# Optimization experiments

Hardware: AMD Instinct MI355X
Metric: run time of the kernel (lower is better)

The kernel has to match this reference:

```python
import jax, jax.numpy as jnp
import numpy as np
from functools import partial

B = 256          # batch_size (== hidden_dim, required by the module's broadcasting)
T = 512          # seq_length
H = 256          # hidden_dim == dim_out
E = 6            # emb_dim
V = 10           # num_input_digits
C = 10           # num_classes


def _kaiming(key, shape):
    fan_in = shape[1]
    return jax.random.normal(key, shape, dtype=jnp.float32) * np.sqrt(2.0 / fan_in)


def setup_inputs() -> dict:
    key = jax.random.key(0)
    ks = jax.random.split(key, 12)
    inp = {
        "x": jax.random.randint(ks[0], (B, T), 0, V),
        "emb": jax.random.normal(ks[1], (V, E), dtype=jnp.float32),
        "Wxg": _kaiming(ks[2], (H, E)), "Whg": _kaiming(ks[3], (H, H)), "bg": jnp.zeros((H,), jnp.float32),
        "Wxi": _kaiming(ks[4], (H, E)), "Whi": _kaiming(ks[5], (H, H)), "bi": jnp.zeros((H,), jnp.float32),
        "Wxf": _kaiming(ks[6], (H, E)), "Whf": _kaiming(ks[7], (H, H)), "bf": jnp.zeros((H,), jnp.float32),
        "Wxo": _kaiming(ks[8], (H, E)), "Who": _kaiming(ks[9], (H, H)), "bo": jnp.zeros((H,), jnp.float32),
        "Wp": _kaiming(ks[10], (C, H)), "bp": jnp.zeros((C,), jnp.float32),
    }
    return inp


def reference(x, emb, Wxg, Whg, bg, Wxi, Whi, bi, Wxf, Whf, bf, Wxo, Who, bo, Wp, bp):
    # x: (B, T) int -> embed -> (B, T, E)
    xe = emb[x]
    # time-major (T, E, B): each step uses x_t.T as in the torch code
    xt_seq = jnp.transpose(xe, (1, 2, 0))

    h0 = jnp.zeros((H, B), jnp.float32)  # h lives as (H, B) per original math
    c0 = jnp.zeros((H, B), jnp.float32)

    def step(carry, xTt):  # xTt: (E, B)
        h, c = carry
        # NOTE: bias (H,) broadcasts over the trailing batch axis (H==B), faithful
        # to the original torch broadcasting.
        g = jnp.tanh(Wxg @ xTt + Whg @ h + bg)
        i = jax.nn.sigmoid(Wxi @ xTt + Whi @ h + bi)
        f = jax.nn.sigmoid(Wxf @ xTt + Whf @ h + bf)
        o = jax.nn.sigmoid(Wxo @ xTt + Who @ h + bo)
        c = g * i + c * f
        h = jnp.tanh(c) * o
        return (h, c), None

    (h, c), _ = jax.lax.scan(step, (h0, c0), xt_seq)
    return (Wp @ h).T + bp  # (B, C)
```

## Files before the change

### kernel.cpp

```cpp
#include <hip/hip_runtime.h>
#include <hip/hip_bf16.h>


typedef __attribute__((ext_vector_type(4))) int   int4v;
typedef __attribute__((ext_vector_type(4))) float float4v;

#define MFMA_I8(a, b, c) __builtin_amdgcn_mfma_i32_16x16x64_i8(a, b, c, 0, 0, 0)

#define K_TANH (-2.8853900817779268f)
#define K_SIG  (-1.4426950408889634f)

#define HSTRIDE 320

__device__ __forceinline__ short f2b(float f) {
    __hip_bfloat16 b = __float2bfloat16(f); return *(short*)&b;
}
__device__ __forceinline__ float b2f(short s) {
    union { unsigned int u; float f; } v; v.u = ((unsigned int)(unsigned short)s) << 16; return v.f;
}
__device__ __forceinline__ float fexp2(float x) {
#if __has_builtin(__builtin_amdgcn_exp2f)
    return __builtin_amdgcn_exp2f(x);
#else
    return __expf(x * 0.6931471805599453f);
#endif
}
__device__ __forceinline__ float frcp(float x) { return __builtin_amdgcn_rcpf(x); }

__global__ __attribute__((amdgpu_flat_work_group_size(1024, 1024), amdgpu_waves_per_eu(4, 4)))
void lstm_i8(
    const int* __restrict__ x,
    const float* __restrict__ emb,
    const float* __restrict__ Wxg, const float* __restrict__ Whg, const float* __restrict__ bg,
    const float* __restrict__ Wxi, const float* __restrict__ Whi, const float* __restrict__ bi,
    const float* __restrict__ Wxf, const float* __restrict__ Whf, const float* __restrict__ bff,
    const float* __restrict__ Wxo, const float* __restrict__ Who, const float* __restrict__ bo,
    const float* __restrict__ Wp, const float* __restrict__ bp,
    float* __restrict__ out)
{
    const int tid = threadIdx.x, bid = blockIdx.x;
    const int c0 = bid * 2;
    const int w = tid >> 6, lane = tid & 63;
    const int l = lane & 15, q = lane >> 4;
    const int col = l & 1;
    const int si  = (l >> 1) & 3;
    const int dup = (l >> 3) & 1;
    const int rw  = 16 * w;
    const int row = rw + 4 * q + si;

    __shared__ __align__(16) unsigned int hbuf[2][2 * HSTRIDE / 4];
    __shared__ __align__(16) short hfin[2 * 264];
    __shared__ unsigned char xdig2[512 * 2];
    __shared__ __align__(16) float tblC[2 * 10 * 1024];
    __shared__ float scaleL[4 * 256];

    const float* WxT[4] = {Wxg, Wxi, Wxf, Wxo};
    const float* WhT[4] = {Whg, Whi, Whf, Who};
    const float* bT[4]  = {bg, bi, bff, bo};

    if (tid < 2 * HSTRIDE / 4) hbuf[0][tid] = 0u;
    if (tid < 1024)
        xdig2[tid] = (unsigned char)x[(c0 + (tid & 1)) * 512 + (tid >> 1)];

    for (int i = tid; i < 5120; i += 1024) {
        int cc  = i / 2560;
        int rem = i - cc * 2560;
        int d = rem >> 8, r = rem & 255;
        float4v v;
        #pragma unroll
        for (int g = 0; g < 4; g++) {
            float s = 0.f;
            #pragma unroll
            for (int e = 0; e < 6; e++) s += WxT[g][r * 6 + e] * emb[d * 6 + e];
            v[g] = (s + bT[g][c0 + cc]) * (g == 0 ? K_TANH : K_SIG);
        }
        *(float4v*)&tblC[cc * 10240 + d * 1024 + r * 4] = v;
    }

    int4v wa[4][4];
    #pragma unroll
    for (int g = 0; g < 4; g++) {
        const float* Wr = WhT[g] + (rw + l) * 256 + q * 16;
        float mx = 0.f;
        #pragma unroll
        for (int kt = 0; kt < 4; kt++)
            #pragma unroll
            for (int c4 = 0; c4 < 4; c4++) {
                float4v v = *(const float4v*)(Wr + kt * 64 + c4 * 4);
                #pragma unroll
                for (int j = 0; j < 4; j++) mx = fmaxf(mx, fabsf(v[j]));
            }
        mx = fmaxf(mx, __shfl_xor(mx, 16));
        mx = fmaxf(mx, __shfl_xor(mx, 32));
        mx = fmaxf(mx, 1e-20f);
        if (q == 0) scaleL[g * 256 + rw + l] = mx;
        float qs = 127.f / mx;
        #pragma unroll
        for (int kt = 0; kt < 4; kt++) {
            int4v f;
            #pragma unroll
            for (int dw = 0; dw < 4; dw++) {
                float4v v = *(const float4v*)(Wr + kt * 64 + dw * 4);
                int word = 0;
                #pragma unroll
                for (int byt = 0; byt < 4; byt++) {
                    int z = (int)rintf(v[byt] * qs);
                    word |= (z & 255) << (8 * byt);
                }
                f[dw] = word;
            }
            wa[g][kt] = f;
        }
    }

    __syncthreads();

    float dscl[4];
    #pragma unroll
    for (int g = 0; g < 4; g++) {
        float kk = (g == 0 ? K_TANH : K_SIG) * (1.f / 16129.f);
        dscl[g] = scaleL[g * 256 + row] * kk;
    }

    const bool bi1 = (si & 1) != 0;
    const bool bi2 = (si & 2) != 0;
    const float* tprow = tblC + col * 10240 + row * 4;
    const int hoff = col * HSTRIDE + row;

    const int4v Z = {0, 0, 0, 0};

    float cs = 0.f, hl = 0.f;

    for (int t = 0; t < 512; t++) {
        const int p = t & 1;
        const char* hbase = (const char*)hbuf[p] + col * HSTRIDE + q * 16;

        int dg = xdig2[t * 2 + col];
        float4v tb = *(const float4v*)(tprow + dg * 1024);

        int4v hf0 = *(const int4v*)(hbase + 0 * 64);
        int4v hf1 = *(const int4v*)(hbase + 1 * 64);
        int4v hf2 = *(const int4v*)(hbase + 2 * 64);
        int4v hf3 = *(const int4v*)(hbase + 3 * 64);

        int4v ag = MFMA_I8(wa[0][0], hf0, Z);
        int4v ai = MFMA_I8(wa[1][0], hf0, Z);
        int4v af = MFMA_I8(wa[2][0], hf0, Z);
        int4v ao = MFMA_I8(wa[3][0], hf0, Z);
        ag = MFMA_I8(wa[0][1], hf1, ag);
        ai = MFMA_I8(wa[1][1], hf1, ai);
        af = MFMA_I8(wa[2][1], hf1, af);
        ao = MFMA_I8(wa[3][1], hf1, ao);
        ag = MFMA_I8(wa[0][2], hf2, ag);
        ai = MFMA_I8(wa[1][2], hf2, ai);
        af = MFMA_I8(wa[2][2], hf2, af);
        ao = MFMA_I8(wa[3][2], hf2, ao);

        ag = MFMA_I8(wa[0][3], hf3, ag);
        int avg_;
        { int s0 = bi1 ? ag[1] : ag[0]; int s1 = bi1 ? ag[3] : ag[2]; avg_ = bi2 ? s1 : s0; }
        float pg = fmaf((float)avg_, dscl[0], tb[0]);
        float Eg = fexp2(pg);

        ai = MFMA_I8(wa[1][3], hf3, ai);
        int avi_;
        { int s0 = bi1 ? ai[1] : ai[0]; int s1 = bi1 ? ai[3] : ai[2]; avi_ = bi2 ? s1 : s0; }
        float pi = fmaf((float)avi_, dscl[1], tb[1]);
        float Ei = fexp2(pi);
        float m1 = (1.f + Eg) * (1.f + Ei);

        af = MFMA_I8(wa[2][3], hf3, af);
        int avf_;
        { int s0 = bi1 ? af[1] : af[0]; int s1 = bi1 ? af[3] : af[2]; avf_ = bi2 ? s1 : s0; }
        float pf = fmaf((float)avf_, dscl[2], tb[2]);
        float Ef = fexp2(pf);
        float fp1 = 1.f + Ef;
        float num = fmaf(cs, m1, (1.f - Eg) * fp1);
        float c   = num * frcp(m1 * fp1);
        cs = c;
        float Ec = fexp2(K_TANH * c);

        ao = MFMA_I8(wa[3][3], hf3, ao);
        int avo_;
        { int s0 = bi1 ? ao[1] : ao[0]; int s1 = bi1 ? ao[3] : ao[2]; avo_ = bi2 ? s1 : s0; }
        float po = fmaf((float)avo_, dscl[3], tb[3]);
        float Eo = fexp2(po);
        float hh = (1.f - Ec) * frcp((1.f + Ec) * (1.f + Eo));
        hl = hh;
        if (dup == 0)
            *((char*)hbuf[1 - p] + hoff) = (char)((int)rintf(hh * 127.f));

        __syncthreads();
    }

    if (dup == 0) hfin[col * 264 + row] = f2b(hl);
    __syncthreads();

    if (tid < 20) {
        int pc = tid / 10, cls = tid - pc * 10;
        const short* hcol = &hfin[pc * 264];
        const float* wrow = Wp + cls * 256;
        float s = 0.f;
        #pragma unroll 8
        for (int k = 0; k < 256; k++) s += b2f(hcol[k]) * wrow[k];
        out[(c0 + pc) * 10 + cls] = s + bp[cls];
    }
}

extern "C" void kernel_launch(void* const* d_in, const int* in_sizes, int n_in,
                              void* d_out, int out_size, void* d_ws, size_t ws_size,
                              hipStream_t stream) {
    const int*   x   = (const int*)d_in[0];
    const float* emb = (const float*)d_in[1];
    const float* Wxg = (const float*)d_in[2];
    const float* Whg = (const float*)d_in[3];
    const float* bg  = (const float*)d_in[4];
    const float* Wxi = (const float*)d_in[5];
    const float* Whi = (const float*)d_in[6];
    const float* bi  = (const float*)d_in[7];
    const float* Wxf = (const float*)d_in[8];
    const float* Whf = (const float*)d_in[9];
    const float* bff = (const float*)d_in[10];
    const float* Wxo = (const float*)d_in[11];
    const float* Who = (const float*)d_in[12];
    const float* bo  = (const float*)d_in[13];
    const float* Wp  = (const float*)d_in[14];
    const float* bp  = (const float*)d_in[15];

    hipLaunchKernelGGL(lstm_i8, dim3(128), dim3(1024), 0, stream,
                       x, emb, Wxg, Whg, bg, Wxi, Whi, bi, Wxf, Whf, bff,
                       Wxo, Who, bo, Wp, bp, (float*)d_out);
}
```

Measured before the change: 553.6 us.

## Halve workgroup to 8 waves with two row tiles per wave, prefetch input table

Each wave now computes two 16-row tiles of the gate matrices, so the block drops from 16 to 8 waves and every lane produces a unique output. The old layout had half the lanes duplicating work. This cuts the number of waves taking part in the per-step barrier and removes the redundant elementwise lanes, in exchange for twice the MFMA chain per wave and twice the weight registers. The next step's input-projection table entry is also loaded ahead of time so its LDS latency overlaps the MFMAs.

```diff
diff --git a/kernel.cpp b/kernel.cpp
--- a/kernel.cpp
+++ b/kernel.cpp
@@ -27,7 +27,7 @@
 }
 __device__ __forceinline__ float frcp(float x) { return __builtin_amdgcn_rcpf(x); }
 
-__global__ __attribute__((amdgpu_flat_work_group_size(1024, 1024), amdgpu_waves_per_eu(4, 4)))
+__global__ __attribute__((amdgpu_flat_work_group_size(512, 512), amdgpu_waves_per_eu(2, 2)))
 void lstm_i8(
     const int* __restrict__ x,
     const float* __restrict__ emb,
@@ -42,11 +42,11 @@
     const int c0 = bid * 2;
     const int w = tid >> 6, lane = tid & 63;
     const int l = lane & 15, q = lane >> 4;
-    const int col = l & 1;
-    const int si  = (l >> 1) & 3;
-    const int dup = (l >> 3) & 1;
-    const int rw  = 16 * w;
-    const int row = rw + 4 * q + si;
+    const int col = lane & 1;
+    const int rtb = (lane >> 1) & 1;
+    const int si  = (lane >> 2) & 3;
+    const int rwb = 32 * w;
+    const int row = rwb + 16 * rtb + 4 * q + si;
 
     __shared__ __align__(16) unsigned int hbuf[2][2 * HSTRIDE / 4];
     __shared__ __align__(16) short hfin[2 * 264];
@@ -59,10 +59,10 @@
     const float* bT[4]  = {bg, bi, bff, bo};
 
     if (tid < 2 * HSTRIDE / 4) hbuf[0][tid] = 0u;
-    if (tid < 1024)
-        xdig2[tid] = (unsigned char)x[(c0 + (tid & 1)) * 512 + (tid >> 1)];
-
-    for (int i = tid; i < 5120; i += 1024) {
+    for (int i = tid; i < 1024; i += 512)
+        xdig2[i] = (unsigned char)x[(c0 + (i & 1)) * 512 + (i >> 1)];
+
+    for (int i = tid; i < 5120; i += 512) {
         int cc  = i / 2560;
         int rem = i - cc * 2560;
         int d = rem >> 8, r = rem & 255;
@@ -77,39 +77,42 @@
         *(float4v*)&tblC[cc * 10240 + d * 1024 + r * 4] = v;
     }
 
-    int4v wa[4][4];
+    int4v wa[2][4][4];
     #pragma unroll
-    for (int g = 0; g < 4; g++) {
-        const float* Wr = WhT[g] + (rw + l) * 256 + q * 16;
-        float mx = 0.f;
+    for (int rt = 0; rt < 2; rt++) {
         #pragma unroll
-        for (int kt = 0; kt < 4; kt++)
+        for (int g = 0; g < 4; g++) {
+            const float* Wr = WhT[g] + (rwb + rt * 16 + l) * 256 + q * 16;
+            float mx = 0.f;
             #pragma unroll
-            for (int c4 = 0; c4 < 4; c4++) {
-                float4v v = *(const float4v*)(Wr + kt * 64 + c4 * 4);
+            for (int kt = 0; kt < 4; kt++)
                 #pragma unroll
-                for (int j = 0; j < 4; j++) mx = fmaxf(mx, fabsf(v[j]));
+                for (int c4 = 0; c4 < 4; c4++) {
+                    float4v v = *(const float4v*)(Wr + kt * 64 + c4 * 4);
+                    #pragma unroll
+                    for (int j = 0; j < 4; j++) mx = fmaxf(mx, fabsf(v[j]));
+                }
+            mx = fmaxf(mx, __shfl_xor(mx, 16));
+            mx = fmaxf(mx, __shfl_xor(mx, 32));
+            mx = fmaxf(mx, 1e-20f);
+            if (q == 0) scaleL[g * 256 + rwb + rt * 16 + l] = mx;
+            float qs = 127.f / mx;
+            #pragma unroll
+            for (int kt = 0; kt < 4; kt++) {
+                int4v f;
+                #pragma unroll
+                for (int dw = 0; dw < 4; dw++) {
+                    float4v v = *(const float4v*)(Wr + kt * 64 + dw * 4);
+                    int word = 0;
+                    #pragma unroll
+                    for (int byt = 0; byt < 4; byt++) {
+                        int z = (int)rintf(v[byt] * qs);
+                        word |= (z & 255) << (8 * byt);
+                    }
+                    f[dw] = word;
+                }
+                wa[rt][g][kt] = f;
             }
-        mx = fmaxf(mx, __shfl_xor(mx, 16));
-        mx = fmaxf(mx, __shfl_xor(mx, 32));
-        mx = fmaxf(mx, 1e-20f);
-        if (q == 0) scaleL[g * 256 + rw + l] = mx;
-        float qs = 127.f / mx;
-        #pragma unroll
-        for (int kt = 0; kt < 4; kt++) {
-            int4v f;
-            #pragma unroll
-            for (int dw = 0; dw < 4; dw++) {
-                float4v v = *(const float4v*)(Wr + kt * 64 + dw * 4);
-                int word = 0;
-                #pragma unroll
-                for (int byt = 0; byt < 4; byt++) {
-                    int z = (int)rintf(v[byt] * qs);
-                    word |= (z & 255) << (8 * byt);
-                }
-                f[dw] = word;
-            }
-            wa[g][kt] = f;
         }
     }
 
@@ -124,54 +127,79 @@
 
     const bool bi1 = (si & 1) != 0;
     const bool bi2 = (si & 2) != 0;
+    const bool brt = rtb != 0;
     const float* tprow = tblC + col * 10240 + row * 4;
     const int hoff = col * HSTRIDE + row;
 
     const int4v Z = {0, 0, 0, 0};
 
     float cs = 0.f, hl = 0.f;
+
+    float4v tb;
+    { int dg = xdig2[0 * 2 + col]; tb = *(const float4v*)(tprow + dg * 1024); }
 
     for (int t = 0; t < 512; t++) {
         const int p = t & 1;
         const char* hbase = (const char*)hbuf[p] + col * HSTRIDE + q * 16;
-
-        int dg = xdig2[t * 2 + col];
-        float4v tb = *(const float4v*)(tprow + dg * 1024);
 
         int4v hf0 = *(const int4v*)(hbase + 0 * 64);
         int4v hf1 = *(const int4v*)(hbase + 1 * 64);
         int4v hf2 = *(const int4v*)(hbase + 2 * 64);
         int4v hf3 = *(const int4v*)(hbase + 3 * 64);
 
-        int4v ag = MFMA_I8(wa[0][0], hf0, Z);
-        int4v ai = MFMA_I8(wa[1][0], hf0, Z);
-        int4v af = MFMA_I8(wa[2][0], hf0, Z);
-        int4v ao = MFMA_I8(wa[3][0], hf0, Z);
-        ag = MFMA_I8(wa[0][1], hf1, ag);
-        ai = MFMA_I8(wa[1][1], hf1, ai);
-        af = MFMA_I8(wa[2][1], hf1, af);
-        ao = MFMA_I8(wa[3][1], hf1, ao);
-        ag = MFMA_I8(wa[0][2], hf2, ag);
-        ai = MFMA_I8(wa[1][2], hf2, ai);
-        af = MFMA_I8(wa[2][2], hf2, af);
-        ao = MFMA_I8(wa[3][2], hf2, ao);
-
-        ag = MFMA_I8(wa[0][3], hf3, ag);
+        int4v ag0 = MFMA_I8(wa[0][0][0], hf0, Z);
+        int4v ag1 = MFMA_I8(wa[1][0][0], hf0, Z);
+        int4v ai0 = MFMA_I8(wa[0][1][0], hf0, Z);
+        int4v ai1 = MFMA_I8(wa[1][1][0], hf0, Z);
+        int4v af0 = MFMA_I8(wa[0][2][0], hf0, Z);
+        int4v af1 = MFMA_I8(wa[1][2][0], hf0, Z);
+        int4v ao0 = MFMA_I8(wa[0][3][0], hf0, Z);
+        int4v ao1 = MFMA_I8(wa[1][3][0], hf0, Z);
+        ag0 = MFMA_I8(wa[0][0][1], hf1, ag0);
+        ag1 = MFMA_I8(wa[1][0][1], hf1, ag1);
+        ai0 = MFMA_I8(wa[0][1][1], hf1, ai0);
+        ai1 = MFMA_I8(wa[1][1][1], hf1, ai1);
+        af0 = MFMA_I8(wa[0][2][1], hf1, af0);
+        af1 = MFMA_I8(wa[1][2][1], hf1, af1);
+        ao0 = MFMA_I8(wa[0][3][1], hf1, ao0);
+        ao1 = MFMA_I8(wa[1][3][1], hf1, ao1);
+        ag0 = MFMA_I8(wa[0][0][2], hf2, ag0);
+        ag1 = MFMA_I8(wa[1][0][2], hf2, ag1);
+        ai0 = MFMA_I8(wa[0][1][2], hf2, ai0);
+        ai1 = MFMA_I8(wa[1][1][2], hf2, ai1);
+        af0 = MFMA_I8(wa[0][2][2], hf2, af0);
+        af1 = MFMA_I8(wa[1][2][2], hf2, af1);
+        ao0 = MFMA_I8(wa[0][3][2], hf2, ao0);
+        ao1 = MFMA_I8(wa[1][3][2], hf2, ao1);
+
+        float4v tbn;
+        { int dgn = xdig2[((t + 1) & 511) * 2 + col]; tbn = *(const float4v*)(tprow + dgn * 1024); }
+
+        ag0 = MFMA_I8(wa[0][0][3], hf3, ag0);
+        ag1 = MFMA_I8(wa[1][0][3], hf3, ag1);
         int avg_;
-        { int s0 = bi1 ? ag[1] : ag[0]; int s1 = bi1 ? ag[3] : ag[2]; avg_ = bi2 ? s1 : s0; }
+        { int t0 = bi1 ? ag0[1] : ag0[0]; int t1 = bi1 ? ag0[3] : ag0[2]; int s0 = bi2 ? t1 : t0;
+          int u0 = bi1 ? ag1[1] : ag1[0]; int u1 = bi1 ? ag1[3] : ag1[2]; int s1 = bi2 ? u1 : u0;
+          avg_ = brt ? s1 : s0; }
         float pg = fmaf((float)avg_, dscl[0], tb[0]);
         float Eg = fexp2(pg);
 
-        ai = MFMA_I8(wa[1][3], hf3, ai);
+        ai0 = MFMA_I8(wa[0][1][3], hf3, ai0);
+        ai1 = MFMA_I8(wa[1][1][3], hf3, ai1);
         int avi_;
-        { int s0 = bi1 ? ai[1] : ai[0]; int s1 = bi1 ? ai[3] : ai[2]; avi_ = bi2 ? s1 : s0; }
+        { int t0 = bi1 ? ai0[1] : ai0[0]; int t1 = bi1 ? ai0[3] : ai0[2]; int s0 = bi2 ? t1 : t0;
+          int u0 = bi1 ? ai1[1] : ai1[0]; int u1 = bi1 ? ai1[3] : ai1[2]; int s1 = bi2 ? u1 : u0;
+          avi_ = brt ? s1 : s0; }
         float pi = fmaf((float)avi_, dscl[1], tb[1]);
         float Ei = fexp2(pi);
         float m1 = (1.f + Eg) * (1.f + Ei);
 
-        af = MFMA_I8(wa[2][3], hf3, af);
+        af0 = MFMA_I8(wa[0][2][3], hf3, af0);
+        af1 = MFMA_I8(wa[1][2][3], hf3, af1);
         int avf_;
-        { int s0 = bi1 ? af[1] : af[0]; int s1 = bi1 ? af[3] : af[2]; avf_ = bi2 ? s1 : s0; }
+        { int t0 = bi1 ? af0[1] : af0[0]; int t1 = bi1 ? af0[3] : af0[2]; int s0 = bi2 ? t1 : t0;
+          int u0 = bi1 ? af1[1] : af1[0]; int u1 = bi1 ? af1[3] : af1[2]; int s1 = bi2 ? u1 : u0;
+          avf_ = brt ? s1 : s0; }
         float pf = fmaf((float)avf_, dscl[2], tb[2]);
         float Ef = fexp2(pf);
         float fp1 = 1.f + Ef;
@@ -180,20 +208,23 @@
         cs = c;
         float Ec = fexp2(K_TANH * c);
 
-        ao = MFMA_I8(wa[3][3], hf3, ao);
+        ao0 = MFMA_I8(wa[0][3][3], hf3, ao0);
+        ao1 = MFMA_I8(wa[1][3][3], hf3, ao1);
         int avo_;
-        { int s0 = bi1 ? ao[1] : ao[0]; int s1 = bi1 ? ao[3] : ao[2]; avo_ = bi2 ? s1 : s0; }
+        { int t0 = bi1 ? ao0[1] : ao0[0]; int t1 = bi1 ? ao0[3] : ao0[2]; int s0 = bi2 ? t1 : t0;
+          int u0 = bi1 ? ao1[1] : ao1[0]; int u1 = bi1 ? ao1[3] : ao1[2]; int s1 = bi2 ? u1 : u0;
+          avo_ = brt ? s1 : s0; }
         float po = fmaf((float)avo_, dscl[3], tb[3]);
         float Eo = fexp2(po);
         float hh = (1.f - Ec) * frcp((1.f + Ec) * (1.f + Eo));
         hl = hh;
-        if (dup == 0)
-            *((char*)hbuf[1 - p] + hoff) = (char)((int)rintf(hh * 127.f));
-
+        *((char*)hbuf[1 - p] + hoff) = (char)((int)rintf(hh * 127.f));
+
+        tb = tbn;
         __syncthreads();
     }
 
-    if (dup == 0) hfin[col * 264 + row] = f2b(hl);
+    hfin[col * 264 + row] = f2b(hl);
     __syncthreads();
 
     if (tid < 20) {
@@ -227,7 +258,7 @@
     const float* Wp  = (const float*)d_in[14];
     const float* bp  = (const float*)d_in[15];
 
-    hipLaunchKernelGGL(lstm_i8, dim3(128), dim3(1024), 0, stream,
+    hipLaunchKernelGGL(lstm_i8, dim3(128), dim3(512), 0, stream,
                        x, emb, Wxg, Whg, bg, Wxi, Whi, bi, Wxf, Whf, bff,
                        Wxo, Who, bo, Wp, bp, (float*)d_out);
 }
```

New measurement: 544.2 us. Within noise of the previous version (-1.7%).
